# Kernel optimization log

Measured on AMD Instinct MI355X. Metric: run time of the kernel, lower is better.

The kernel has to match this reference:

```python
import jax, jax.numpy as jnp
import numpy as np

B, S, E, H = 4, 2048, 1024, 16
D = E // H  # head_dim = 64

def setup_inputs() -> dict:
    key = jax.random.key(0)
    ks = jax.random.split(key, 9)
    std = 1.0 / np.sqrt(E)
    return {
        "x":  jax.random.normal(ks[0], (B, S, E), jnp.float32),
        "Wq": jax.random.uniform(ks[1], (E, E), jnp.float32, -std, std),
        "bq": jax.random.uniform(ks[2], (E,),   jnp.float32, -std, std),
        "Wk": jax.random.uniform(ks[3], (E, E), jnp.float32, -std, std),
        "bk": jax.random.uniform(ks[4], (E,),   jnp.float32, -std, std),
        "Wv": jax.random.uniform(ks[5], (E, E), jnp.float32, -std, std),
        "bv": jax.random.uniform(ks[6], (E,),   jnp.float32, -std, std),
        "Wo": jax.random.uniform(ks[7], (E, E), jnp.float32, -std, std),
        "bo": jax.random.uniform(ks[8], (E,),   jnp.float32, -std, std),
    }

def reference(x, Wq, bq, Wk, bk, Wv, bv, Wo, bo):
    b, s, e = x.shape
    # QKV projections (weights stored as [in,out] == torch W.T applied as x @ W)
    q = (x @ Wq + bq).reshape(b, s, H, D).transpose(0, 2, 1, 3)  # [B,H,S,D]
    k = (x @ Wk + bk).reshape(b, s, H, D).transpose(0, 2, 1, 3)
    v = (x @ Wv + bv).reshape(b, s, H, D).transpose(0, 2, 1, 3)
    scores = jnp.einsum('bhqd,bhkd->bhqk', q, k) / jnp.sqrt(jnp.float32(D))
    causal = jnp.triu(jnp.ones((s, s), bool), k=1)  # True above diagonal
    scores = jnp.where(causal, -jnp.inf, scores)
    p = jax.nn.softmax(scores, axis=-1)  # dropout disabled (eval mode)
    out = jnp.einsum('bhqk,bhkd->bhqd', p, v)  # [B,H,S,D]
    out = out.transpose(0, 2, 1, 3).reshape(b, s, e)
    return out @ Wo + bo
```

## Files before the change

kernel.cpp:

```cpp
#include <hip/hip_runtime.h>
#include <math.h>

#define E_DIM 1024
#define B_DIM 4
#define S_DIM 2048
#define H_DIM 16
#define D_HEAD 64
#define M_DIM (B_DIM * S_DIM)
#define LOG2E 1.44269504f
#define RESCALE_THR 4.0f

typedef _Float16 half8 __attribute__((ext_vector_type(8)));
typedef _Float16 half4 __attribute__((ext_vector_type(4)));
typedef __fp16  fp16x2 __attribute__((ext_vector_type(2)));
typedef float floatx4 __attribute__((ext_vector_type(4)));
typedef unsigned uint2v __attribute__((ext_vector_type(2)));
#define MFMA_F16(a, b, c) __builtin_amdgcn_mfma_f32_16x16x32_f16(a, b, c, 0, 0, 0)

#if __has_builtin(__builtin_amdgcn_exp2f)
#define EXP2F(x) __builtin_amdgcn_exp2f(x)
#else
#define EXP2F(x) exp2f(x)
#endif

union H4 { fp16x2 h2[2]; half4 h4; };
union H8 { fp16x2 h2[4]; half8 h8; };

__device__ inline float red_xor16(float x, int lane) {
#if __has_builtin(__builtin_amdgcn_permlane16_swap)
    uint2v r = __builtin_amdgcn_permlane16_swap(
        __builtin_bit_cast(unsigned, x), __builtin_bit_cast(unsigned, x), false, false);
    return __builtin_bit_cast(float, (lane & 16) ? r[0] : r[1]);
#else
    return __shfl_xor(x, 16);
#endif
}
__device__ inline float red_xor32(float x, int lane) {
#if __has_builtin(__builtin_amdgcn_permlane32_swap)
    uint2v r = __builtin_amdgcn_permlane32_swap(
        __builtin_bit_cast(unsigned, x), __builtin_bit_cast(unsigned, x), false, false);
    return __builtin_bit_cast(float, (lane & 32) ? r[0] : r[1]);
#else
    return __shfl_xor(x, 32);
#endif
}

#define GLDS16(g, l)                                                          \
    __builtin_amdgcn_global_load_lds(                                         \
        (const __attribute__((address_space(1))) void*)(g),                   \
        (__attribute__((address_space(3))) void*)(l), 16, 0, 0)

__device__ const int SEG_QBLK[40] = {3,4,5,6,7,7,8,8,9,9,10,10,11,11,11,12,12,12,
                                     13,13,13,14,14,14,15,15,15,15,
                                     2,6,10,14, 1,5,9,13, 0,4,8,12};
__device__ const int SEG_SEG[40]  = {0,0,0,0,0,1,0,1,0,1,0,1,0,1,2,0,1,2,
                                     0,1,2,0,1,2,0,1,2,3,
                                     0,1,2,3, 0,1,2,3, 0,1,2,3};
__device__ const int SEG_BASE[16] = {0,1,2,3,4,6,8,10,12,15,18,21,24,28,32,36};

__global__ __launch_bounds__(256) void cvt_x(
    const float* __restrict__ X, _Float16* __restrict__ Xh)
{
    size_t i = ((size_t)blockIdx.x * 256 + threadIdx.x) * 8;
    float4 a = *(const float4*)&X[i];
    float4 b = *(const float4*)&X[i + 4];
    half8 h = {(_Float16)a.x, (_Float16)a.y, (_Float16)a.z, (_Float16)a.w,
               (_Float16)b.x, (_Float16)b.y, (_Float16)b.z, (_Float16)b.w};
    *(half8*)&Xh[i] = h;
}

__global__ __launch_bounds__(256) void cvt_w(
    const float* __restrict__ W0, const float* __restrict__ W1,
    const float* __restrict__ W2, const float* __restrict__ W3,
    _Float16* __restrict__ T0, _Float16* __restrict__ T1,
    _Float16* __restrict__ T2, _Float16* __restrict__ T3)
{
    const int z = blockIdx.z;
    const float* W = (z == 0) ? W0 : (z == 1) ? W1 : (z == 2) ? W2 : W3;
    _Float16*   T  = (z == 0) ? T0 : (z == 1) ? T1 : (z == 2) ? T2 : T3;
    const int k0 = blockIdx.x * 64, n0 = blockIdx.y * 64;
    const int tid = threadIdx.x;
    __shared__ float t[64][65];
#pragma unroll
    for (int it = 0; it < 4; it++) {
        int r = it * 16 + (tid >> 4);
        int c = (tid & 15) * 4;
        float4 v = *(const float4*)&W[(size_t)(k0 + r) * E_DIM + n0 + c];
        t[r][c] = v.x; t[r][c + 1] = v.y; t[r][c + 2] = v.z; t[r][c + 3] = v.w;
    }
    __syncthreads();
#pragma unroll
    for (int it = 0; it < 2; it++) {
        int n = it * 32 + (tid >> 3);
        int kk = (tid & 7) * 8;
        half8 h;
#pragma unroll
        for (int j = 0; j < 8; j++) h[j] = (_Float16)t[kk + j][n];
        *(half8*)&T[(size_t)(n0 + n) * E_DIM + k0 + kk] = h;
    }
}

#define GEMM_CORE(Aptr, Bptr)                                                 \
    const int tid = threadIdx.x;                                              \
    const int wave = tid >> 6, lane = tid & 63;                               \
    const int m16 = lane & 15, quad = lane >> 4;                              \
    const int wm = (wave >> 1) * 64, wn = (wave & 1) * 64;                    \
    const int m0 = blockIdx.x * 128, n0 = blockIdx.y * 128;                   \
    __shared__ _Float16 As[128 * 32];                                         \
    __shared__ _Float16 Bs[128 * 32];                                         \
    floatx4 acc[4][4];                                                        \
    const floatx4 zf = {0.f, 0.f, 0.f, 0.f};                                  \
    _Pragma("unroll") for (int i = 0; i < 4; i++)                             \
        _Pragma("unroll") for (int j = 0; j < 4; j++) acc[i][j] = zf;         \
    const int lrow = lane >> 2, lseg = lane & 3;                              \
    const _Float16* gA = (Aptr) + (size_t)(m0 + wave * 32 + lrow) * E_DIM + lseg * 8; \
    const _Float16* gB = (Bptr) + (size_t)(n0 + wave * 32 + lrow) * E_DIM + lseg * 8; \
    _Float16* lA = As + (wave * 32) * 32;                                     \
    _Float16* lB = Bs + (wave * 32) * 32;                                     \
    for (int k0 = 0; k0 < E_DIM; k0 += 32) {                                  \
        __syncthreads();                                                      \
        GLDS16(gA + k0, lA);                                                  \
        GLDS16(gA + 16 * E_DIM + k0, lA + 16 * 32);                           \
        GLDS16(gB + k0, lB);                                                  \
        GLDS16(gB + 16 * E_DIM + k0, lB + 16 * 32);                           \
        __syncthreads();                                                      \
        half8 af[4], bf[4];                                                   \
        _Pragma("unroll") for (int mt = 0; mt < 4; mt++)                      \
            af[mt] = *(const half8*)&As[(wm + mt * 16 + m16) * 32 + quad * 8];\
        _Pragma("unroll") for (int nt = 0; nt < 4; nt++)                      \
            bf[nt] = *(const half8*)&Bs[(wn + nt * 16 + m16) * 32 + quad * 8];\
        _Pragma("unroll") for (int mt = 0; mt < 4; mt++)                      \
            _Pragma("unroll") for (int nt = 0; nt < 4; nt++)                  \
                acc[mt][nt] = MFMA_F16(af[mt], bf[nt], acc[mt][nt]);          \
    }

#define STAGE256(t, s)                                                        \
    _Pragma("unroll") for (int i = 0; i < 4; i++) {                           \
        GLDS16(aS[i] + (t) * 64, As + (s) * 16384 + dOff[i]);                 \
        GLDS16(bS[i] + (t) * 64, Bs + (s) * 16384 + dOff[i]);                 \
    }

#define PH_READ_A(mh)                                                         \
    _Pragma("unroll") for (int am = 0; am < 4; am++)                          \
        _Pragma("unroll") for (int kh = 0; kh < 2; kh++)                      \
            a_[am][kh] = *(const half8*)&As[sb +                              \
                (wr * 128 + (mh) * 64 + am * 16 + m16) * 64 +                 \
                (((kh * 4 + quad) ^ sw8) * 8)];

#define PH_READ_B(nh)                                                         \
    _Pragma("unroll") for (int bn = 0; bn < 2; bn++)                          \
        _Pragma("unroll") for (int kh = 0; kh < 2; kh++)                      \
            b_[bn][kh] = *(const half8*)&Bs[sb +                              \
                (wc * 64 + (nh) * 32 + bn * 16 + m16) * 64 +                  \
                (((kh * 4 + quad) ^ sw8) * 8)];

#define PH_MFMA(mh, nh)                                                       \
    __builtin_amdgcn_s_setprio(1);                                            \
    _Pragma("unroll") for (int am = 0; am < 4; am++)                          \
        _Pragma("unroll") for (int bn = 0; bn < 2; bn++)                      \
            acc[(mh) * 4 + am][(nh) * 2 + bn] =                               \
                MFMA_F16(a_[am][1], b_[bn][1],                                \
                    MFMA_F16(a_[am][0], b_[bn][0],                            \
                             acc[(mh) * 4 + am][(nh) * 2 + bn]));             \
    __builtin_amdgcn_s_setprio(0);

#define GEMM256_CORE(Aptr, Bptr)                                              \
    const int tid = threadIdx.x;                                              \
    const int wave = tid >> 6, lane = tid & 63;                               \
    const int m16 = lane & 15, quad = lane >> 4;                              \
    const int wr = wave >> 2, wc = wave & 3;                                  \
    const int m0 = blockIdx.x * 256, n0 = blockIdx.y * 256;                   \
    const int sw8 = m16 & 7;                                                  \
    __shared__ _Float16 As[2 * 16384];                                        \
    __shared__ _Float16 Bs[2 * 16384];                                        \
    floatx4 acc[8][4];                                                        \
    const floatx4 zf = {0.f, 0.f, 0.f, 0.f};                                  \
    _Pragma("unroll") for (int i = 0; i < 8; i++)                             \
        _Pragma("unroll") for (int j = 0; j < 4; j++) acc[i][j] = zf;         \
    const _Float16* aS[4];                                                    \
    const _Float16* bS[4];                                                    \
    int dOff[4];                                                              \
    _Pragma("unroll") for (int i = 0; i < 4; i++) {                           \
        int u = i * 512 + tid;                                                \
        int ru = u >> 3, cblk = (u & 7) ^ (ru & 7);                           \
        aS[i] = (Aptr) + (size_t)(m0 + ru) * E_DIM + cblk * 8;                \
        bS[i] = (Bptr) + (size_t)(n0 + ru) * E_DIM + cblk * 8;                \
        dOff[i] = i * 4096 + wave * 512;                                      \
    }                                                                         \
    STAGE256(0, 0);                                                           \
    STAGE256(1, 1);                                                           \
    asm volatile("s_waitcnt vmcnt(8)" ::: "memory");                          \
    __builtin_amdgcn_s_barrier();                                             \
    half8 a_[4][2], b_[2][2];                                                 \
    for (int t = 0; t < 16; t++) {                                            \
        const int sb = (t & 1) * 16384;                                       \
        PH_READ_A(0); PH_READ_B(0); PH_MFMA(0, 0);                            \
        PH_READ_B(1); PH_MFMA(0, 1);                                          \
        PH_READ_A(1); PH_MFMA(1, 1);                                          \
        PH_READ_B(0); PH_MFMA(1, 0);                                          \
        if (t + 1 < 16) {                                                     \
            asm volatile("s_waitcnt lgkmcnt(0)" ::: "memory");                \
            __builtin_amdgcn_s_barrier();                                     \
            if (t + 2 < 16) {                                                 \
                STAGE256(t + 2, t & 1);                                       \
                asm volatile("s_waitcnt vmcnt(8)" ::: "memory");              \
            } else {                                                          \
                asm volatile("s_waitcnt vmcnt(0)" ::: "memory");              \
            }                                                                 \
            __builtin_amdgcn_s_barrier();                                     \
        }                                                                     \
    }

__global__ __launch_bounds__(512) void qkv_mfma(
    const _Float16* __restrict__ Xh,
    const _Float16* __restrict__ Tq, const float* __restrict__ bq,
    const _Float16* __restrict__ Tk, const float* __restrict__ bk,
    const _Float16* __restrict__ Tv, const float* __restrict__ bv,
    _Float16* __restrict__ Qo, _Float16* __restrict__ Ko, _Float16* __restrict__ Vo)
{
    const int z = blockIdx.z;
    const _Float16* Wt   = (z == 0) ? Tq : (z == 1) ? Tk : Tv;
    const float*    bias = (z == 0) ? bq : (z == 1) ? bk : bv;

    GEMM256_CORE(Xh, Wt)

    if (z == 2) {
#pragma unroll
        for (int nt = 0; nt < 4; nt++) {
            int n = n0 + wc * 64 + nt * 16 + m16;
            int h = n >> 6, d = n & 63;
            int dt = d >> 4, ld = d & 15;
            float bias_v = bias[n];
#pragma unroll
            for (int mt = 0; mt < 8; mt++) {
                int m_b = m0 + wr * 128 + mt * 16 + quad * 4;
                int b = m_b >> 11, s = m_b & 2047;
                int bh = b * H_DIM + h;
                int c = s >> 6, kl = s & 63;
                int kh = kl >> 5, q8 = (kl >> 2) & 3, j0 = ((kl >> 4) & 1) * 4;
                size_t off = ((size_t)bh * 32 + c) * 4096
                           + (size_t)(((dt * 2 + kh) * 64 + q8 * 16 + ld) * 8 + j0);
                half4 hv;
#pragma unroll
                for (int r = 0; r < 4; r++) hv[r] = (_Float16)(acc[mt][nt][r] + bias_v);
                *(half4*)&Vo[off] = hv;
            }
        }
    } else {
        _Float16* Out = (z == 0) ? Qo : Ko;
        const float sc = (z == 0) ? 0.125f * LOG2E : 1.0f;
#pragma unroll
        for (int nt = 0; nt < 4; nt++) {
            int n = n0 + wc * 64 + nt * 16 + m16;
            int h = n >> 6, d = n & 63;
            int dh = d >> 5, qd = (d >> 3) & 3, j = d & 7;
            float bias_v = bias[n];
#pragma unroll
            for (int mt = 0; mt < 8; mt++) {
#pragma unroll
                for (int r = 0; r < 4; r++) {
                    int m = m0 + wr * 128 + mt * 16 + quad * 4 + r;
                    int b = m >> 11, s = m & 2047;
                    int bh = b * H_DIM + h;
                    size_t off;
                    if (z == 0) {
                        int qblk = s >> 7, qq = s & 127;
                        int sub = qq >> 4, lq = qq & 15;
                        off = ((size_t)bh * 16 + qblk) * 8192
                            + (size_t)(((sub * 2 + dh) * 64 + qd * 16 + lq) * 8 + j);
                    } else {
                        int c = s >> 6, kl = s & 63;
                        int kt = kl >> 4, lk = kl & 15;
                        off = ((size_t)bh * 32 + c) * 4096
                            + (size_t)(((kt * 2 + dh) * 64 + qd * 16 + lk) * 8 + j);
                    }
                    Out[off] = (_Float16)((acc[mt][nt][r] + bias_v) * sc);
                }
            }
        }
    }
}

__global__ __launch_bounds__(256) void out_mfma(
    const _Float16* __restrict__ Oh, const _Float16* __restrict__ To,
    const float* __restrict__ bias, float* __restrict__ Out)
{
    GEMM_CORE(Oh, To)

#pragma unroll
    for (int nt = 0; nt < 4; nt++) {
        int n = n0 + wn + nt * 16 + m16;
        float bias_v = bias[n];
#pragma unroll
        for (int mt = 0; mt < 4; mt++) {
#pragma unroll
            for (int r = 0; r < 4; r++) {
                int m = m0 + wm + mt * 16 + quad * 4 + r;
                Out[(size_t)m * E_DIM + n] = acc[mt][nt][r] + bias_v;
            }
        }
    }
}

__global__ __launch_bounds__(64) void attn_mfma(
    const _Float16* __restrict__ Qb, const _Float16* __restrict__ Kb,
    const _Float16* __restrict__ Vb, _Float16* __restrict__ Opart,
    float* __restrict__ Mv, float* __restrict__ Lv, _Float16* __restrict__ O)
{
    const int L = blockIdx.x;
    const int xcd = L & 7;
    const int u = L >> 3;
    const int bh = xcd * 8 + (u / 160);
    const int su = u % 160;
    const int wid = su >> 2;
    const int wave = su & 3;
    const int qblk = SEG_QBLK[wid];
    const int seg  = SEG_SEG[wid];
    const int q0 = qblk * 128;
    const int c0 = seg * 8;
    const int c1 = min(c0 + 8, 2 * qblk + 2);
    const bool solo = (c0 == 0) && (c1 == 2 * qblk + 2);
    const int lane = threadIdx.x;
    const int m16 = lane & 15, quad = lane >> 4;

    const int qmin = q0 + wave * 32;
    const int qmax = qmin + 31;
    const int c1w = min(c1, (qmax >> 6) + 1);

    const _Float16* gQ = Qb + ((size_t)bh * 16 + qblk) * 8192 + wave * 2048 + lane * 8;
    half8 qf[2][2];
#pragma unroll
    for (int mt = 0; mt < 2; mt++)
#pragma unroll
        for (int dh = 0; dh < 2; dh++)
            qf[mt][dh] = *(const half8*)&gQ[(mt * 2 + dh) * 512];

    float m_i[2] = {-INFINITY, -INFINITY}, l_i[2] = {0.f, 0.f};
    floatx4 acco[2][4];
    const floatx4 zf = {0.f, 0.f, 0.f, 0.f};
#pragma unroll
    for (int mt = 0; mt < 2; mt++)
#pragma unroll
        for (int dt = 0; dt < 4; dt++) acco[mt][dt] = zf;

    const _Float16* gK = Kb + ((size_t)bh * 32 + c0) * 4096 + lane * 8;
    const _Float16* gV = Vb + ((size_t)bh * 32 + c0) * 4096 + lane * 8;

    half8 kf[4][2];
#pragma unroll
    for (int kt = 0; kt < 4; kt++)
#pragma unroll
        for (int dh = 0; dh < 2; dh++)
            kf[kt][dh] = *(const half8*)&gK[(kt * 2 + dh) * 512];
    gK += 4096;

    for (int c = c0; c < c1w; c++) {
        const int k0 = c * 64;

        half8 vf[4][2];
#pragma unroll
        for (int dt = 0; dt < 4; dt++)
#pragma unroll
            for (int kh = 0; kh < 2; kh++)
                vf[dt][kh] = *(const half8*)&gV[(dt * 2 + kh) * 512];
        gV += 4096;

        floatx4 sf[2][4];
        __builtin_amdgcn_s_setprio(1);
#pragma unroll
        for (int kt = 0; kt < 4; kt++)
#pragma unroll
            for (int mt = 0; mt < 2; mt++)
                sf[mt][kt] = MFMA_F16(kf[kt][1], qf[mt][1],
                               MFMA_F16(kf[kt][0], qf[mt][0], zf));
        __builtin_amdgcn_s_setprio(0);

        if (c + 1 < c1w) {
#pragma unroll
            for (int kt = 0; kt < 4; kt++)
#pragma unroll
                for (int dh = 0; dh < 2; dh++)
                    kf[kt][dh] = *(const half8*)&gK[(kt * 2 + dh) * 512];
            gK += 4096;
        }

        const bool full = (k0 + 63 <= qmin);
#pragma unroll
        for (int mt = 0; mt < 2; mt++) {
            const int qg = qmin + mt * 16 + m16;
#pragma unroll
            for (int kt = 0; kt < 4; kt++)
#pragma unroll
                for (int r = 0; r < 4; r++) {
                    if (!full) {
                        int key = k0 + kt * 16 + quad * 4 + r;
                        if (key > qg) sf[mt][kt][r] = -INFINITY;
                    }
                }
            float mk[4];
#pragma unroll
            for (int kt = 0; kt < 4; kt++)
                mk[kt] = fmaxf(fmaxf(sf[mt][kt][0], sf[mt][kt][1]),
                               fmaxf(sf[mt][kt][2], sf[mt][kt][3]));
            float mx = fmaxf(fmaxf(mk[0], mk[1]), fmaxf(mk[2], mk[3]));
            mx = fmaxf(mx, red_xor16(mx, lane));
            mx = fmaxf(mx, red_xor32(mx, lane));

            float mn = m_i[mt];
            if (!__all(mx <= mn + RESCALE_THR)) {
                mn = fmaxf(mn, mx);
                float alpha = EXP2F(m_i[mt] - mn);
                m_i[mt] = mn;
                l_i[mt] *= alpha;
#pragma unroll
                for (int dt = 0; dt < 4; dt++) acco[mt][dt] *= alpha;
            }

            float ls = 0.f;
            H8 u8[2];
#pragma unroll
            for (int kt = 0; kt < 4; kt++) {
                float e0 = EXP2F(sf[mt][kt][0] - mn);
                float e1 = EXP2F(sf[mt][kt][1] - mn);
                float e2 = EXP2F(sf[mt][kt][2] - mn);
                float e3 = EXP2F(sf[mt][kt][3] - mn);
                ls += (e0 + e1) + (e2 + e3);
                u8[kt >> 1].h2[(kt & 1) * 2]     = __builtin_amdgcn_cvt_pkrtz(e0, e1);
                u8[kt >> 1].h2[(kt & 1) * 2 + 1] = __builtin_amdgcn_cvt_pkrtz(e2, e3);
            }
            ls += red_xor16(ls, lane);
            ls += red_xor32(ls, lane);
            l_i[mt] += ls;

            __builtin_amdgcn_s_setprio(1);
#pragma unroll
            for (int dt = 0; dt < 4; dt++)
                acco[mt][dt] = MFMA_F16(vf[dt][1], u8[1].h8,
                                 MFMA_F16(vf[dt][0], u8[0].h8, acco[mt][dt]));
            __builtin_amdgcn_s_setprio(0);
        }
    }

    if (solo) {
        const int b = bh >> 4;
        const int h = bh & (H_DIM - 1);
#pragma unroll
        for (int mt = 0; mt < 2; mt++) {
            float inv = 1.f / l_i[mt];
            int q = qmin + mt * 16 + m16;
            _Float16* dst = O + (size_t)(b * S_DIM + q) * E_DIM + h * 64;
#pragma unroll
            for (int dt = 0; dt < 4; dt++) {
                H4 u4;
                u4.h2[0] = __builtin_amdgcn_cvt_pkrtz(acco[mt][dt][0] * inv, acco[mt][dt][1] * inv);
                u4.h2[1] = __builtin_amdgcn_cvt_pkrtz(acco[mt][dt][2] * inv, acco[mt][dt][3] * inv);
                *(half4*)&dst[dt * 16 + quad * 4] = u4.h4;
            }
        }
    } else {
        const size_t prow = ((size_t)bh * 40 + SEG_BASE[qblk] + seg) * 128;
#pragma unroll
        for (int mt = 0; mt < 2; mt++) {
            int lq = wave * 32 + mt * 16 + m16;
            if (quad == 0) {
                Mv[prow + lq] = m_i[mt];
                Lv[prow + lq] = l_i[mt];
            }
            _Float16* dst = Opart + (prow + lq) * 64;
#pragma unroll
            for (int dt = 0; dt < 4; dt++) {
                H4 u4;
                u4.h2[0] = __builtin_amdgcn_cvt_pkrtz(acco[mt][dt][0], acco[mt][dt][1]);
                u4.h2[1] = __builtin_amdgcn_cvt_pkrtz(acco[mt][dt][2], acco[mt][dt][3]);
                *(half4*)&dst[dt * 16 + quad * 4] = u4.h4;
            }
        }
    }
}

__global__ __launch_bounds__(256) void attn_combine(
    const _Float16* __restrict__ Opart, const float* __restrict__ Mv,
    const float* __restrict__ Lv, _Float16* __restrict__ O)
{
    const int qb = blockIdx.x + 4, bh = blockIdx.y;
    const int nseg = (qb >> 2) + 1;
    const size_t pbase = ((size_t)bh * 40 + SEG_BASE[qb]) * 128;
    const int t = threadIdx.x;
    const int r = t >> 1, dh = (t & 1) * 32;

    float m_s[4], w[4];
    float M = -INFINITY;
    for (int s = 0; s < nseg; s++) {
        m_s[s] = Mv[pbase + s * 128 + r];
        M = fmaxf(M, m_s[s]);
    }
    float L = 0.f;
    for (int s = 0; s < nseg; s++) {
        w[s] = EXP2F(m_s[s] - M);
        L += Lv[pbase + s * 128 + r] * w[s];
    }
    const float invL = 1.f / L;

    const int b = bh >> 4, h = bh & (H_DIM - 1);
    const int q = qb * 128 + r;
    _Float16* dst = O + (size_t)(b * S_DIM + q) * E_DIM + h * 64 + dh;
#pragma unroll
    for (int d0 = 0; d0 < 32; d0 += 8) {
        float acc[8] = {0.f, 0.f, 0.f, 0.f, 0.f, 0.f, 0.f, 0.f};
        for (int s = 0; s < nseg; s++) {
            half8 v = *(const half8*)&Opart[(pbase + s * 128 + r) * 64 + dh + d0];
#pragma unroll
            for (int j = 0; j < 8; j++) acc[j] += w[s] * (float)v[j];
        }
        half8 o;
#pragma unroll
        for (int j = 0; j < 8; j++) o[j] = (_Float16)(acc[j] * invL);
        *(half8*)&dst[d0] = o;
    }
}

extern "C" void kernel_launch(void* const* d_in, const int* in_sizes, int n_in,
                              void* d_out, int out_size, void* d_ws, size_t ws_size,
                              hipStream_t stream) {
    const float* x  = (const float*)d_in[0];
    const float* Wq = (const float*)d_in[1];
    const float* bq = (const float*)d_in[2];
    const float* Wk = (const float*)d_in[3];
    const float* bk = (const float*)d_in[4];
    const float* Wv = (const float*)d_in[5];
    const float* bv = (const float*)d_in[6];
    const float* Wo = (const float*)d_in[7];
    const float* bo = (const float*)d_in[8];

    const size_t SZ = (size_t)M_DIM * E_DIM;
    const size_t WZ = (size_t)E_DIM * E_DIM;
    _Float16* Xh = (_Float16*)d_ws;
    _Float16* Tq = Xh + SZ;
    _Float16* Tk = Tq + WZ;
    _Float16* Tv = Tk + WZ;
    _Float16* To = Tv + WZ;
    _Float16* Qb = To + WZ;
    _Float16* Kb = Qb + SZ;
    _Float16* Vb = Kb + SZ;
    _Float16* Opart = Vb + SZ;
    float* Mv = (float*)(Opart + (size_t)2560 * 8192);
    float* Lv = Mv + 2560 * 128;
    _Float16* Oh = Xh;

    cvt_x<<<dim3(M_DIM * E_DIM / 2048), 256, 0, stream>>>(x, Xh);
    cvt_w<<<dim3(16, 16, 4), 256, 0, stream>>>(Wq, Wk, Wv, Wo, Tq, Tk, Tv, To);

    qkv_mfma<<<dim3(M_DIM / 256, E_DIM / 256, 3), 512, 0, stream>>>(
        Xh, Tq, bq, Tk, bk, Tv, bv, Qb, Kb, Vb);

    attn_mfma<<<dim3(8 * 8 * 160), 64, 0, stream>>>(
        Qb, Kb, Vb, Opart, Mv, Lv, Oh);

    attn_combine<<<dim3(12, B_DIM * H_DIM), 256, 0, stream>>>(Opart, Mv, Lv, Oh);

    out_mfma<<<dim3(M_DIM / 128, E_DIM / 128), 256, 0, stream>>>(
        Oh, To, bo, (float*)d_out);
}
```

Baseline: 299.5 us.

## Split attention work into 16-query waves packed four per block

Measured after the change: 309.2 us. 1.03x slower.

```diff
diff --git a/kernel.cpp b/kernel.cpp
--- a/kernel.cpp
+++ b/kernel.cpp
@@ -302,7 +302,7 @@
     }
 }
 
-__global__ __launch_bounds__(64) void attn_mfma(
+__global__ __launch_bounds__(256) void attn_mfma(
     const _Float16* __restrict__ Qb, const _Float16* __restrict__ Kb,
     const _Float16* __restrict__ Vb, _Float16* __restrict__ Opart,
     float* __restrict__ Mv, float* __restrict__ Lv, _Float16* __restrict__ O)
@@ -310,38 +310,33 @@
     const int L = blockIdx.x;
     const int xcd = L & 7;
     const int u = L >> 3;
-    const int bh = xcd * 8 + (u / 160);
-    const int su = u % 160;
-    const int wid = su >> 2;
-    const int wave = su & 3;
+    const int bh = xcd * 8 + (u / 80);
+    const int g = u % 80;
+    const int su = g * 4 + (threadIdx.x >> 6);
+    const int wid = su >> 3;
+    const int w8 = su & 7;
     const int qblk = SEG_QBLK[wid];
     const int seg  = SEG_SEG[wid];
     const int q0 = qblk * 128;
     const int c0 = seg * 8;
     const int c1 = min(c0 + 8, 2 * qblk + 2);
     const bool solo = (c0 == 0) && (c1 == 2 * qblk + 2);
-    const int lane = threadIdx.x;
+    const int lane = threadIdx.x & 63;
     const int m16 = lane & 15, quad = lane >> 4;
 
-    const int qmin = q0 + wave * 32;
-    const int qmax = qmin + 31;
-    const int c1w = min(c1, (qmax >> 6) + 1);
-
-    const _Float16* gQ = Qb + ((size_t)bh * 16 + qblk) * 8192 + wave * 2048 + lane * 8;
-    half8 qf[2][2];
-#pragma unroll
-    for (int mt = 0; mt < 2; mt++)
-#pragma unroll
-        for (int dh = 0; dh < 2; dh++)
-            qf[mt][dh] = *(const half8*)&gQ[(mt * 2 + dh) * 512];
-
-    float m_i[2] = {-INFINITY, -INFINITY}, l_i[2] = {0.f, 0.f};
-    floatx4 acco[2][4];
+    const int qmin = q0 + w8 * 16;
+    const int c1w = min(c1, ((qmin + 15) >> 6) + 1);
+
+    const _Float16* gQ = Qb + ((size_t)bh * 16 + qblk) * 8192 + w8 * 1024 + lane * 8;
+    half8 qf[2];
+    qf[0] = *(const half8*)&gQ[0];
+    qf[1] = *(const half8*)&gQ[512];
+
+    float m_i = -INFINITY, l_i = 0.f;
+    floatx4 acco[4];
     const floatx4 zf = {0.f, 0.f, 0.f, 0.f};
 #pragma unroll
-    for (int mt = 0; mt < 2; mt++)
-#pragma unroll
-        for (int dt = 0; dt < 4; dt++) acco[mt][dt] = zf;
+    for (int dt = 0; dt < 4; dt++) acco[dt] = zf;
 
     const _Float16* gK = Kb + ((size_t)bh * 32 + c0) * 4096 + lane * 8;
     const _Float16* gV = Vb + ((size_t)bh * 32 + c0) * 4096 + lane * 8;
@@ -365,14 +360,12 @@
                 vf[dt][kh] = *(const half8*)&gV[(dt * 2 + kh) * 512];
         gV += 4096;
 
-        floatx4 sf[2][4];
+        floatx4 sf[4];
         __builtin_amdgcn_s_setprio(1);
 #pragma unroll
         for (int kt = 0; kt < 4; kt++)
-#pragma unroll
-            for (int mt = 0; mt < 2; mt++)
-                sf[mt][kt] = MFMA_F16(kf[kt][1], qf[mt][1],
-                               MFMA_F16(kf[kt][0], qf[mt][0], zf));
+            sf[kt] = MFMA_F16(kf[kt][1], qf[1],
+                       MFMA_F16(kf[kt][0], qf[0], zf));
         __builtin_amdgcn_s_setprio(0);
 
         if (c + 1 < c1w) {
@@ -385,95 +378,86 @@
         }
 
         const bool full = (k0 + 63 <= qmin);
-#pragma unroll
-        for (int mt = 0; mt < 2; mt++) {
-            const int qg = qmin + mt * 16 + m16;
-#pragma unroll
-            for (int kt = 0; kt < 4; kt++)
-#pragma unroll
-                for (int r = 0; r < 4; r++) {
-                    if (!full) {
-                        int key = k0 + kt * 16 + quad * 4 + r;
-                        if (key > qg) sf[mt][kt][r] = -INFINITY;
-                    }
+        const int qg = qmin + m16;
+#pragma unroll
+        for (int kt = 0; kt < 4; kt++)
+#pragma unroll
+            for (int r = 0; r < 4; r++) {
+                if (!full) {
+                    int key = k0 + kt * 16 + quad * 4 + r;
+                    if (key > qg) sf[kt][r] = -INFINITY;
                 }
-            float mk[4];
-#pragma unroll
-            for (int kt = 0; kt < 4; kt++)
-                mk[kt] = fmaxf(fmaxf(sf[mt][kt][0], sf[mt][kt][1]),
-                               fmaxf(sf[mt][kt][2], sf[mt][kt][3]));
-            float mx = fmaxf(fmaxf(mk[0], mk[1]), fmaxf(mk[2], mk[3]));
-            mx = fmaxf(mx, red_xor16(mx, lane));
-            mx = fmaxf(mx, red_xor32(mx, lane));
-
-            float mn = m_i[mt];
-            if (!__all(mx <= mn + RESCALE_THR)) {
-                mn = fmaxf(mn, mx);
-                float alpha = EXP2F(m_i[mt] - mn);
-                m_i[mt] = mn;
-                l_i[mt] *= alpha;
-#pragma unroll
-                for (int dt = 0; dt < 4; dt++) acco[mt][dt] *= alpha;
             }
-
-            float ls = 0.f;
-            H8 u8[2];
-#pragma unroll
-            for (int kt = 0; kt < 4; kt++) {
-                float e0 = EXP2F(sf[mt][kt][0] - mn);
-                float e1 = EXP2F(sf[mt][kt][1] - mn);
-                float e2 = EXP2F(sf[mt][kt][2] - mn);
-                float e3 = EXP2F(sf[mt][kt][3] - mn);
-                ls += (e0 + e1) + (e2 + e3);
-                u8[kt >> 1].h2[(kt & 1) * 2]     = __builtin_amdgcn_cvt_pkrtz(e0, e1);
-                u8[kt >> 1].h2[(kt & 1) * 2 + 1] = __builtin_amdgcn_cvt_pkrtz(e2, e3);
-            }
-            ls += red_xor16(ls, lane);
-            ls += red_xor32(ls, lane);
-            l_i[mt] += ls;
-
-            __builtin_amdgcn_s_setprio(1);
-#pragma unroll
-            for (int dt = 0; dt < 4; dt++)
-                acco[mt][dt] = MFMA_F16(vf[dt][1], u8[1].h8,
-                                 MFMA_F16(vf[dt][0], u8[0].h8, acco[mt][dt]));
-            __builtin_amdgcn_s_setprio(0);
-        }
+        float mk[4];
+#pragma unroll
+        for (int kt = 0; kt < 4; kt++)
+            mk[kt] = fmaxf(fmaxf(sf[kt][0], sf[kt][1]),
+                           fmaxf(sf[kt][2], sf[kt][3]));
+        float mx = fmaxf(fmaxf(mk[0], mk[1]), fmaxf(mk[2], mk[3]));
+        mx = fmaxf(mx, red_xor16(mx, lane));
+        mx = fmaxf(mx, red_xor32(mx, lane));
+
+        float mn = m_i;
+        if (!__all(mx <= mn + RESCALE_THR)) {
+            mn = fmaxf(mn, mx);
+            float alpha = EXP2F(m_i - mn);
+            m_i = mn;
+            l_i *= alpha;
+#pragma unroll
+            for (int dt = 0; dt < 4; dt++) acco[dt] *= alpha;
+        }
+
+        float ls = 0.f;
+        H8 u8[2];
+#pragma unroll
+        for (int kt = 0; kt < 4; kt++) {
+            float e0 = EXP2F(sf[kt][0] - mn);
+            float e1 = EXP2F(sf[kt][1] - mn);
+            float e2 = EXP2F(sf[kt][2] - mn);
+            float e3 = EXP2F(sf[kt][3] - mn);
+            ls += (e0 + e1) + (e2 + e3);
+            u8[kt >> 1].h2[(kt & 1) * 2]     = __builtin_amdgcn_cvt_pkrtz(e0, e1);
+            u8[kt >> 1].h2[(kt & 1) * 2 + 1] = __builtin_amdgcn_cvt_pkrtz(e2, e3);
+        }
+        ls += red_xor16(ls, lane);
+        ls += red_xor32(ls, lane);
+        l_i += ls;
+
+        __builtin_amdgcn_s_setprio(1);
+#pragma unroll
+        for (int dt = 0; dt < 4; dt++)
+            acco[dt] = MFMA_F16(vf[dt][1], u8[1].h8,
+                         MFMA_F16(vf[dt][0], u8[0].h8, acco[dt]));
+        __builtin_amdgcn_s_setprio(0);
     }
 
     if (solo) {
         const int b = bh >> 4;
         const int h = bh & (H_DIM - 1);
-#pragma unroll
-        for (int mt = 0; mt < 2; mt++) {
-            float inv = 1.f / l_i[mt];
-            int q = qmin + mt * 16 + m16;
-            _Float16* dst = O + (size_t)(b * S_DIM + q) * E_DIM + h * 64;
-#pragma unroll
-            for (int dt = 0; dt < 4; dt++) {
-                H4 u4;
-                u4.h2[0] = __builtin_amdgcn_cvt_pkrtz(acco[mt][dt][0] * inv, acco[mt][dt][1] * inv);
-                u4.h2[1] = __builtin_amdgcn_cvt_pkrtz(acco[mt][dt][2] * inv, acco[mt][dt][3] * inv);
-                *(half4*)&dst[dt * 16 + quad * 4] = u4.h4;
-            }
+        float inv = 1.f / l_i;
+        int q = qmin + m16;
+        _Float16* dst = O + (size_t)(b * S_DIM + q) * E_DIM + h * 64;
+#pragma unroll
+        for (int dt = 0; dt < 4; dt++) {
+            H4 u4;
+            u4.h2[0] = __builtin_amdgcn_cvt_pkrtz(acco[dt][0] * inv, acco[dt][1] * inv);
+            u4.h2[1] = __builtin_amdgcn_cvt_pkrtz(acco[dt][2] * inv, acco[dt][3] * inv);
+            *(half4*)&dst[dt * 16 + quad * 4] = u4.h4;
         }
     } else {
         const size_t prow = ((size_t)bh * 40 + SEG_BASE[qblk] + seg) * 128;
-#pragma unroll
-        for (int mt = 0; mt < 2; mt++) {
-            int lq = wave * 32 + mt * 16 + m16;
-            if (quad == 0) {
-                Mv[prow + lq] = m_i[mt];
-                Lv[prow + lq] = l_i[mt];
-            }
-            _Float16* dst = Opart + (prow + lq) * 64;
-#pragma unroll
-            for (int dt = 0; dt < 4; dt++) {
-                H4 u4;
-                u4.h2[0] = __builtin_amdgcn_cvt_pkrtz(acco[mt][dt][0], acco[mt][dt][1]);
-                u4.h2[1] = __builtin_amdgcn_cvt_pkrtz(acco[mt][dt][2], acco[mt][dt][3]);
-                *(half4*)&dst[dt * 16 + quad * 4] = u4.h4;
-            }
+        int lq = w8 * 16 + m16;
+        if (quad == 0) {
+            Mv[prow + lq] = m_i;
+            Lv[prow + lq] = l_i;
+        }
+        _Float16* dst = Opart + (prow + lq) * 64;
+#pragma unroll
+        for (int dt = 0; dt < 4; dt++) {
+            H4 u4;
+            u4.h2[0] = __builtin_amdgcn_cvt_pkrtz(acco[dt][0], acco[dt][1]);
+            u4.h2[1] = __builtin_amdgcn_cvt_pkrtz(acco[dt][2], acco[dt][3]);
+            *(half4*)&dst[dt * 16 + quad * 4] = u4.h4;
         }
     }
 }
@@ -553,7 +537,7 @@
     qkv_mfma<<<dim3(M_DIM / 256, E_DIM / 256, 3), 512, 0, stream>>>(
         Xh, Tq, bq, Tk, bk, Tv, bv, Qb, Kb, Vb);
 
-    attn_mfma<<<dim3(8 * 8 * 160), 64, 0, stream>>>(
+    attn_mfma<<<dim3(8 * 8 * 80), 256, 0, stream>>>(
         Qb, Kb, Vb, Opart, Mv, Lv, Oh);
 
     attn_combine<<<dim3(12, B_DIM * H_DIM), 256, 0, stream>>>(Opart, Mv, Lv, Oh);
```
